# Optimization experiments

Hardware: AMD Instinct MI355X
Metric: run time of the kernel (lower is better)

The kernel has to match this reference:

```python
import jax, jax.numpy as jnp
import numpy as np

D = 1280          # hidden_size
NH = 16           # num_heads
HD = 80           # head_dim
DEPTH = 4         # number of vision blocks
INTER = 3420      # mlp intermediate size
MERGE = 2         # spatial_merge_size
OUT = 3584        # merger out_hidden_size
GRID = (1, 40, 40)  # (t, h, w) patch grid -> 1600 tokens
N = GRID[0] * GRID[1] * GRID[2]
PATCH_IN = 3 * 2 * 14 * 14  # in_channels * temporal_patch * patch^2 = 1176


def _pos_emb():
    """Deterministic vision RoPE cos/sin per Qwen2_5_VLVisionModel.rot_pos_emb."""
    t, h, w = GRID
    mh, mw = h // MERGE, w // MERGE
    intra = np.arange(MERGE)
    row = np.arange(mh)[:, None, None, None] * MERGE + intra[None, None, :, None]
    col = np.arange(mw)[None, :, None, None] * MERGE + intra[None, None, None, :]
    row = np.broadcast_to(row, (mh, mw, MERGE, MERGE)).reshape(-1)
    col = np.broadcast_to(col, (mh, mw, MERGE, MERGE)).reshape(-1)
    pos = np.stack([row, col], axis=-1)        # (h*w, 2)
    if t > 1:
        pos = np.tile(pos, (t, 1))
    rot_dim = HD // 2                          # 40
    inv = 1.0 / (10000.0 ** (np.arange(0, rot_dim, 2, dtype=np.float64) / rot_dim))
    table = np.outer(np.arange(max(h, w)), inv)        # (max_hw, rot_dim//2)
    rpe = table[pos].reshape(pos.shape[0], -1)         # (N, rot_dim)
    emb = np.concatenate([rpe, rpe], axis=-1)          # (N, HD)
    return np.cos(emb).astype(np.float32), np.sin(emb).astype(np.float32)


def setup_inputs() -> dict:
    key = jax.random.key(0)
    ks = iter(jax.random.split(key, 40))
    def w(shape, s=0.02):
        return jax.random.normal(next(ks), shape, jnp.float32) * s
    cos, sin = _pos_emb()
    return dict(
        pixel_values=w((N, PATCH_IN), 1.0),
        cos=jnp.asarray(cos), sin=jnp.asarray(sin),
        patch_w=w((D, PATCH_IN)),                       # Conv3d stride==kernel -> linear
        norm1_w=jnp.ones((DEPTH, D), jnp.float32),
        qkv_w=w((DEPTH, 3 * D, D)), qkv_b=jnp.zeros((DEPTH, 3 * D), jnp.float32),
        proj_w=w((DEPTH, D, D)), proj_b=jnp.zeros((DEPTH, D), jnp.float32),
        norm2_w=jnp.ones((DEPTH, D), jnp.float32),
        gate_w=w((DEPTH, INTER, D)), gate_b=jnp.zeros((DEPTH, INTER), jnp.float32),
        up_w=w((DEPTH, INTER, D)), up_b=jnp.zeros((DEPTH, INTER), jnp.float32),
        down_w=w((DEPTH, D, INTER)), down_b=jnp.zeros((DEPTH, D), jnp.float32),
        lnq_w=jnp.ones((D,), jnp.float32),
        m1_w=w((D * MERGE ** 2, D * MERGE ** 2)), m1_b=jnp.zeros((D * MERGE ** 2,), jnp.float32),
        m2_w=w((OUT, D * MERGE ** 2)), m2_b=jnp.zeros((OUT,), jnp.float32),
    )


def _rms(x, w, eps=1e-6):
    return x * jax.lax.rsqrt(jnp.mean(x * x, axis=-1, keepdims=True) + eps) * w


def _rotate_half(x):
    x1, x2 = jnp.split(x, 2, axis=-1)
    return jnp.concatenate([-x2, x1], axis=-1)


def _forward(pixel_values, cos, sin, patch_w, norm1_w, qkv_w, qkv_b, proj_w, proj_b,
             norm2_w, gate_w, gate_b, up_w, up_b, down_w, down_b,
             lnq_w, m1_w, m1_b, m2_w, m2_b):
    # patch embed: Conv3d with kernel==stride collapses to a linear projection
    x = pixel_values @ patch_w.T                       # (N, D)
    c = cos[:, None, :]                                # (N, 1, HD)
    s = sin[:, None, :]
    scale = HD ** -0.5
    for i in range(DEPTH):
        # --- attention ---
        h = _rms(x, norm1_w[i])
        qkv = (h @ qkv_w[i].T + qkv_b[i]).reshape(N, 3, NH, HD)
        q, k, v = qkv[:, 0], qkv[:, 1], qkv[:, 2]      # (N, NH, HD)
        q = q * c + _rotate_half(q) * s
        k = k * c + _rotate_half(k) * s
        # NOTE: this impl applies NO cu_seqlens window mask -> full dense attention
        aw = jnp.einsum('nhd,mhd->hnm', q, k) * scale  # (NH, N, N)
        aw = jax.nn.softmax(aw.astype(jnp.float32), axis=-1).astype(x.dtype)
        o = jnp.einsum('hnm,mhd->nhd', aw, v).reshape(N, D)
        x = x + o @ proj_w[i].T + proj_b[i]
        # --- mlp (SwiGLU) ---
        h = _rms(x, norm2_w[i])
        g = h @ gate_w[i].T + gate_b[i]
        u = h @ up_w[i].T + up_b[i]
        x = x + (jax.nn.silu(g) * u) @ down_w[i].T + down_b[i]
    # --- patch merger ---
    h = _rms(x, lnq_w).reshape(-1, D * MERGE ** 2)      # (N/4, 5120)
    h = jax.nn.gelu(h @ m1_w.T + m1_b, approximate=False)
    return h @ m2_w.T + m2_b                            # (N/4, OUT)


def reference(pixel_values, cos, sin, patch_w, norm1_w, qkv_w, qkv_b, proj_w, proj_b,
              norm2_w, gate_w, gate_b, up_w, up_b, down_w, down_b,
              lnq_w, m1_w, m1_b, m2_w, m2_b):
    return _forward(pixel_values, cos, sin, patch_w, norm1_w, qkv_w, qkv_b, proj_w,
                    proj_b, norm2_w, gate_w, gate_b, up_w, up_b, down_w, down_b,
                    lnq_w, m1_w, m1_b, m2_w, m2_b)
```

## Files before the change

### kernel.cpp

```cpp
#include <hip/hip_runtime.h>


typedef __bf16 bf16x8 __attribute__((ext_vector_type(8)));
typedef float  f32x4  __attribute__((ext_vector_type(4)));
typedef unsigned short u16;

#define DEV __device__ __forceinline__

DEV u16 f2bf(float f) {
    union { float f; unsigned u; } v; v.f = f;
    unsigned r = v.u + 0x7FFFu + ((v.u >> 16) & 1u);
    return (u16)(r >> 16);
}
DEV float bf2f(u16 b) {
    union { float f; unsigned u; } v; v.u = ((unsigned)b) << 16; return v.f;
}

DEV void gload16(const u16* g, u16* l) {
    __builtin_amdgcn_global_load_lds(
        (const __attribute__((address_space(1))) unsigned int*)g,
        (__attribute__((address_space(3))) unsigned int*)l, 16, 0, 0);
}

enum { EPI_NONE = 0, EPI_BIAS = 1, EPI_BIAS_RESID = 2, EPI_BIAS_GELU = 3, EPI_PART = 4 };

DEV unsigned xcd_map(unsigned lin, unsigned nwg) {
    unsigned q = nwg >> 3, r = nwg & 7, xc = lin & 7, off = lin >> 3;
    return (xc < r ? xc * (q + 1) : r * (q + 1) + (xc - r) * q) + off;
}

__global__ void cvt_kernel(const float* __restrict__ src, u16* __restrict__ dst,
                           int Rs, int Cs, int Rp, int Cp,
                           long long sls, long long dls)
{
    const float* s = src + (size_t)blockIdx.y * sls;
    u16* d = dst + (size_t)blockIdx.y * dls;
    int idx = blockIdx.x * 256 + threadIdx.x;
    int cpc = Cp >> 3;
    if (idx >= Rp * cpc) return;
    int row = idx / cpc;
    int c0  = (idx - row * cpc) * 8;
    u16 v[8];
    if (row < Rs && c0 + 8 <= Cs) {
        float4 a = *reinterpret_cast<const float4*>(&s[(size_t)row * Cs + c0]);
        float4 b = *reinterpret_cast<const float4*>(&s[(size_t)row * Cs + c0 + 4]);
        v[0] = f2bf(a.x); v[1] = f2bf(a.y); v[2] = f2bf(a.z); v[3] = f2bf(a.w);
        v[4] = f2bf(b.x); v[5] = f2bf(b.y); v[6] = f2bf(b.z); v[7] = f2bf(b.w);
    } else {
#pragma unroll
        for (int j = 0; j < 8; ++j) {
            int c = c0 + j;
            v[j] = (row < Rs && c < Cs) ? f2bf(s[(size_t)row * Cs + c]) : (u16)0;
        }
    }
    *reinterpret_cast<uint4*>(&d[(size_t)row * Cp + c0]) =
        *reinterpret_cast<const uint4*>(v);
}

__global__ void gub_kernel(const float* __restrict__ gb, const float* __restrict__ ub,
                           float* __restrict__ dst)
{
    int i = blockIdx.x * 256 + threadIdx.x;
    if (i >= 4 * 6912) return;
    int l = i / 6912, c = i - l * 6912;
    float v = 0.f;
    if (c < 3456) { if (c < 3420) v = gb[l * 3420 + c]; }
    else { int c2 = c - 3456; if (c2 < 3420) v = ub[l * 3420 + c2]; }
    dst[i] = v;
}

template <int EPI, bool OF32>
__global__ __launch_bounds__(256, 3)
void gemm16_kernel(const u16* __restrict__ A, const u16* __restrict__ B,
                   const float* __restrict__ bias, const float* __restrict__ resid,
                   void* __restrict__ outp, int Kp, int ldc, int Rlim,
                   int ktn, size_t zstride)
{
    __shared__ u16 sA[3][4096];
    __shared__ u16 sB[3][4096];
    const int tid  = threadIdx.x;
    const int lane = tid & 63;
    const int w    = tid >> 6;

    const unsigned gy  = gridDim.y;
    const unsigned nwg = gridDim.x * gy;
    const unsigned lin = blockIdx.x + blockIdx.y * gridDim.x;
    const unsigned id2 = xcd_map(lin, nwg);
    const int c0 = (int)(id2 / gy) * 128;
    const int r0 = (int)(id2 - (id2 / gy) * gy) * 128;

    const int wr  = (w >> 1) * 64;
    const int wc  = (w & 1) * 64;
    const int l15 = lane & 15;
    const int kk  = (lane >> 4) * 8;
    const int pco = (((lane >> 4) ^ ((l15 >> 1) & 3)) * 8) - kk;

    const int ca  = w * 128 + lane;
    const int cb  = ca + 64;
    const int sza = ((ca & 3) ^ ((ca >> 3) & 3)) * 8;
    const int szb = ((cb & 3) ^ ((cb >> 3) & 3)) * 8;
    const size_t arow0 = (size_t)(r0 + (ca >> 2)) * Kp + sza;
    const size_t brow0 = (size_t)(c0 + (ca >> 2)) * Kp + sza;
    const size_t arow1 = (size_t)(r0 + (cb >> 2)) * Kp + szb;
    const size_t brow1 = (size_t)(c0 + (cb >> 2)) * Kp + szb;

    f32x4 acc[4][4];
#pragma unroll
    for (int i = 0; i < 4; ++i)
#pragma unroll
        for (int j = 0; j < 4; ++j) acc[i][j] = (f32x4){0.f, 0.f, 0.f, 0.f};

    const int kt0 = blockIdx.z * ktn;
    auto stage = [&](int kt, int buf) {
        int k0 = kt * 32;
        gload16(A + arow0 + k0, &sA[buf][ca * 8]);
        gload16(B + brow0 + k0, &sB[buf][ca * 8]);
        gload16(A + arow1 + k0, &sA[buf][cb * 8]);
        gload16(B + brow1 + k0, &sB[buf][cb * 8]);
    };
    auto compute = [&](int buf) {
        bf16x8 af[4], bfr[4];
#pragma unroll
        for (int f = 0; f < 4; ++f) {
            af[f]  = *reinterpret_cast<const bf16x8*>(&sA[buf][(wr + f * 16 + l15) * 32 + kk + pco]);
            bfr[f] = *reinterpret_cast<const bf16x8*>(&sB[buf][(wc + f * 16 + l15) * 32 + kk + pco]);
        }
#pragma unroll
        for (int fr = 0; fr < 4; ++fr)
#pragma unroll
            for (int fc = 0; fc < 4; ++fc)
                acc[fr][fc] = __builtin_amdgcn_mfma_f32_16x16x32_bf16(af[fr], bfr[fc], acc[fr][fc], 0, 0, 0);
    };

    const int NT = ktn;
    stage(kt0, 0);
    if (NT > 1) stage(kt0 + 1, 1);
    int bcur = 0;
    for (int t = 0; t < NT - 1; ++t) {
        asm volatile("s_waitcnt vmcnt(4)" ::: "memory");
        __builtin_amdgcn_s_barrier();
        __builtin_amdgcn_sched_barrier(0);
        if (t + 2 < NT) {
            int bn = bcur + 2; if (bn >= 3) bn -= 3;
            stage(kt0 + t + 2, bn);
        }
        __builtin_amdgcn_sched_barrier(0);
        compute(bcur);
        bcur = (bcur == 2) ? 0 : bcur + 1;
    }
    asm volatile("s_waitcnt vmcnt(0)" ::: "memory");
    __builtin_amdgcn_s_barrier();
    __builtin_amdgcn_sched_barrier(0);
    compute(bcur);

    const int rowb = r0 + wr + (lane >> 4) * 4;
    const int colb = c0 + wc + l15;
    if (EPI == EPI_PART) {
        float* pp = (float*)outp + (size_t)blockIdx.z * zstride;
#pragma unroll
        for (int fc = 0; fc < 4; ++fc) {
            int col = colb + fc * 16;
#pragma unroll
            for (int fr = 0; fr < 4; ++fr)
#pragma unroll
                for (int r2 = 0; r2 < 4; ++r2)
                    pp[(size_t)(rowb + fr * 16 + r2) * ldc + col] = acc[fr][fc][r2];
        }
        return;
    }
#pragma unroll
    for (int fc = 0; fc < 4; ++fc) {
        int col = colb + fc * 16;
        float bv = (EPI != EPI_NONE) ? bias[col] : 0.f;
#pragma unroll
        for (int fr = 0; fr < 4; ++fr) {
#pragma unroll
            for (int r2 = 0; r2 < 4; ++r2) {
                int row = rowb + fr * 16 + r2;
                if (row >= Rlim) continue;
                float v = acc[fr][fc][r2] + bv;
                if (EPI == EPI_BIAS_RESID) v += resid[(size_t)row * ldc + col];
                if (EPI == EPI_BIAS_GELU)  v = 0.5f * v * (1.f + erff(v * 0.70710678118f));
                if (OF32) ((float*)outp)[(size_t)row * ldc + col] = v;
                else      ((u16*)outp)[(size_t)row * ldc + col] = f2bf(v);
            }
        }
    }
}

template <int EPI, bool OF32>
__global__ __launch_bounds__(256, 4)
void gemm32_kernel(const u16* __restrict__ A, const u16* __restrict__ B,
                   const float* __restrict__ bias, const float* __restrict__ resid,
                   void* __restrict__ outp, int Kp, int ldc, int Rlim)
{
    __shared__ u16 sA[3][1024];
    __shared__ u16 sB[3][4096];
    const int tid  = threadIdx.x;
    const int lane = tid & 63;
    const int w    = tid >> 6;

    const unsigned gy  = gridDim.y;
    const unsigned nwg = gridDim.x * gy;
    const unsigned lin = blockIdx.x + blockIdx.y * gridDim.x;
    const unsigned id2 = xcd_map(lin, nwg);
    const int c0 = (int)(id2 / gy) * 128;
    const int r0 = (int)(id2 - (id2 / gy) * gy) * 32;

    const int wc  = w * 32;
    const int l15 = lane & 15;
    const int kk  = (lane >> 4) * 8;
    const int pco = (((lane >> 4) ^ ((l15 >> 1) & 3)) * 8) - kk;

    const int cB0 = tid, cB1 = tid + 256, cA = tid & 127;
    const size_t bsrc0 = (size_t)(c0 + (cB0 >> 2)) * Kp + ((cB0 & 3) ^ ((cB0 >> 3) & 3)) * 8;
    const size_t bsrc1 = (size_t)(c0 + (cB1 >> 2)) * Kp + ((cB1 & 3) ^ ((cB1 >> 3) & 3)) * 8;
    const size_t asrc  = (size_t)(r0 + (cA  >> 2)) * Kp + ((cA  & 3) ^ ((cA  >> 3) & 3)) * 8;

    f32x4 acc[2][2];
#pragma unroll
    for (int i = 0; i < 2; ++i)
#pragma unroll
        for (int j = 0; j < 2; ++j) acc[i][j] = (f32x4){0.f, 0.f, 0.f, 0.f};

    auto stage = [&](int kt, int buf) {
        int k0 = kt * 32;
        gload16(B + bsrc0 + k0, &sB[buf][cB0 * 8]);
        gload16(B + bsrc1 + k0, &sB[buf][cB1 * 8]);
        gload16(A + asrc  + k0, &sA[buf][cA * 8]);
    };
    auto compute = [&](int buf) {
        bf16x8 af[2], bfr[2];
#pragma unroll
        for (int f = 0; f < 2; ++f) {
            af[f]  = *reinterpret_cast<const bf16x8*>(&sA[buf][(f * 16 + l15) * 32 + kk + pco]);
            bfr[f] = *reinterpret_cast<const bf16x8*>(&sB[buf][(wc + f * 16 + l15) * 32 + kk + pco]);
        }
#pragma unroll
        for (int fr = 0; fr < 2; ++fr)
#pragma unroll
            for (int fc = 0; fc < 2; ++fc)
                acc[fr][fc] = __builtin_amdgcn_mfma_f32_16x16x32_bf16(af[fr], bfr[fc], acc[fr][fc], 0, 0, 0);
    };

    const int NT = Kp >> 5;
    stage(0, 0);
    stage(1, 1);
    int bcur = 0;
    for (int t = 0; t < NT - 1; ++t) {
        asm volatile("s_waitcnt vmcnt(3)" ::: "memory");
        __builtin_amdgcn_s_barrier();
        __builtin_amdgcn_sched_barrier(0);
        if (t + 2 < NT) {
            int bn = bcur + 2; if (bn >= 3) bn -= 3;
            stage(t + 2, bn);
        }
        __builtin_amdgcn_sched_barrier(0);
        compute(bcur);
        bcur = (bcur == 2) ? 0 : bcur + 1;
    }
    asm volatile("s_waitcnt vmcnt(0)" ::: "memory");
    __builtin_amdgcn_s_barrier();
    __builtin_amdgcn_sched_barrier(0);
    compute(bcur);

    const int rowb = r0 + (lane >> 4) * 4;
    const int colb = c0 + wc + l15;
#pragma unroll
    for (int fc = 0; fc < 2; ++fc) {
        int col = colb + fc * 16;
        float bv = (EPI != EPI_NONE) ? bias[col] : 0.f;
#pragma unroll
        for (int fr = 0; fr < 2; ++fr) {
#pragma unroll
            for (int r2 = 0; r2 < 4; ++r2) {
                int row = rowb + fr * 16 + r2;
                if (row >= Rlim) continue;
                float v = acc[fr][fc][r2] + bv;
                if (EPI == EPI_BIAS_RESID) v += resid[(size_t)row * ldc + col];
                if (EPI == EPI_BIAS_GELU)  v = 0.5f * v * (1.f + erff(v * 0.70710678118f));
                if (OF32) ((float*)outp)[(size_t)row * ldc + col] = v;
                else      ((u16*)outp)[(size_t)row * ldc + col] = f2bf(v);
            }
        }
    }
}

template <int GELU, bool OF32>
__global__ void reduce_kernel(const float* __restrict__ part, const float* __restrict__ bias,
                              void* __restrict__ outp, int C, int S, size_t zstride, int total4)
{
    int i = blockIdx.x * 256 + threadIdx.x;
    if (i >= total4) return;
    int cq = C >> 2;
    int rr = i / cq;
    int cc = (i - rr * cq) * 4;
    size_t bidx = (size_t)rr * C + cc;
    float4 s = *reinterpret_cast<const float4*>(&part[bidx]);
    for (int z = 1; z < S; ++z) {
        float4 p = *reinterpret_cast<const float4*>(&part[z * zstride + bidx]);
        s.x += p.x; s.y += p.y; s.z += p.z; s.w += p.w;
    }
    float4 b = *reinterpret_cast<const float4*>(&bias[cc]);
    s.x += b.x; s.y += b.y; s.z += b.z; s.w += b.w;
    if (GELU) {
        s.x = 0.5f * s.x * (1.f + erff(s.x * 0.70710678118f));
        s.y = 0.5f * s.y * (1.f + erff(s.y * 0.70710678118f));
        s.z = 0.5f * s.z * (1.f + erff(s.z * 0.70710678118f));
        s.w = 0.5f * s.w * (1.f + erff(s.w * 0.70710678118f));
    }
    if (OF32) {
        *reinterpret_cast<float4*>(&((float*)outp)[bidx]) = s;
    } else {
        u16 v[4] = { f2bf(s.x), f2bf(s.y), f2bf(s.z), f2bf(s.w) };
        *reinterpret_cast<uint2*>(&((u16*)outp)[bidx]) = *reinterpret_cast<const uint2*>(v);
    }
}

__global__ void rms_kernel(const float* __restrict__ x, const float* __restrict__ w,
                           u16* __restrict__ out, int cols)
{
    const int row = blockIdx.x;
    const int tid = threadIdx.x;
    const float* xr = x + (size_t)row * cols;
    float ss = 0.f;
    for (int c = tid; c < cols; c += 256) { float v = xr[c]; ss += v * v; }
#pragma unroll
    for (int m = 1; m < 64; m <<= 1) ss += __shfl_xor(ss, m);
    __shared__ float wsum[4];
    if ((tid & 63) == 0) wsum[tid >> 6] = ss;
    __syncthreads();
    float tot = wsum[0] + wsum[1] + wsum[2] + wsum[3];
    float rs = rsqrtf(tot / (float)cols + 1e-6f);
    u16* orow = out + (size_t)row * cols;
    for (int c = tid; c < cols; c += 256) orow[c] = f2bf(xr[c] * rs * w[c]);
}

__global__ void rope_kernel(u16* __restrict__ qkv, const float* __restrict__ cosb,
                            const float* __restrict__ sinb)
{
    int idx = blockIdx.x * 256 + threadIdx.x;
    int n   = idx / 640;
    int rem = idx - n * 640;
    int hh  = rem / 40;
    int d   = rem - hh * 40;
    float c0 = cosb[n * 80 + d];
    float s0 = sinb[n * 80 + d];
    float c1 = cosb[n * 80 + d + 40];
    float s1 = sinb[n * 80 + d + 40];
    size_t base = (size_t)n * 3840 + hh * 80;
    float a = bf2f(qkv[base + d]), b = bf2f(qkv[base + d + 40]);
    qkv[base + d]      = f2bf(a * c0 - b * s0);
    qkv[base + d + 40] = f2bf(b * c1 + a * s1);
    base += 1280;
    a = bf2f(qkv[base + d]); b = bf2f(qkv[base + d + 40]);
    qkv[base + d]      = f2bf(a * c0 - b * s0);
    qkv[base + d + 40] = f2bf(b * c1 + a * s1);
}

__global__ void silu_mul_kernel(const u16* __restrict__ gu, u16* __restrict__ outb)
{
    int idx = blockIdx.x * 256 + threadIdx.x;
    if (idx >= 1664 * 432) return;
    int row = idx / 432, c8 = (idx - row * 432) * 8;
    u16 gv[8], uv[8];
    *reinterpret_cast<uint4*>(gv) = *reinterpret_cast<const uint4*>(&gu[(size_t)row * 6912 + c8]);
    *reinterpret_cast<uint4*>(uv) = *reinterpret_cast<const uint4*>(&gu[(size_t)row * 6912 + 3456 + c8]);
#pragma unroll
    for (int j = 0; j < 8; ++j) {
        float x = bf2f(gv[j]);
        gv[j] = f2bf(x / (1.f + expf(-x)) * bf2f(uv[j]));
    }
    *reinterpret_cast<uint4*>(&outb[(size_t)row * 3456 + c8]) = *reinterpret_cast<const uint4*>(gv);
}

__global__ __launch_bounds__(256, 2)
void attn_kernel(const u16* __restrict__ qkv, u16* __restrict__ o)
{
    __shared__ __align__(16) u16 Klds[64][104];
    __shared__ __align__(16) u16 Vt[80][72];
    __shared__ __align__(16) u16 Plds[4][16][72];
    const int tid  = threadIdx.x;
    const int lane = tid & 63;
    const int w    = tid >> 6;
    const int l15  = lane & 15;
    const int kk   = (lane >> 4) * 8;
    unsigned lin = blockIdx.y * 25 + blockIdx.x;
    unsigned id2 = (lin & 7) * 50 + (lin >> 3);
    const int hh = (int)(id2 / 25);
    const int qt = (int)(id2 - hh * 25);
    const float scale = 0.11180339887498949f;

    const int qrow = qt * 64 + w * 16 + l15;
    bf16x8 aq[3];
#pragma unroll
    for (int s = 0; s < 3; ++s) {
        int d = 32 * s + kk;
        union { bf16x8 v; uint4 q; } uu;
        if (d < 80) uu.q = *reinterpret_cast<const uint4*>(&qkv[(size_t)qrow * 3840 + hh * 80 + d]);
        else        uu.q = (uint4){0u, 0u, 0u, 0u};
        aq[s] = uu.v;
    }

    f32x4 acc_o[5];
#pragma unroll
    for (int fd = 0; fd < 5; ++fd) acc_o[fd] = (f32x4){0.f, 0.f, 0.f, 0.f};
    float m[4], lsum[4];
#pragma unroll
    for (int r2 = 0; r2 < 4; ++r2) { m[r2] = -__builtin_inff(); lsum[r2] = 0.f; }

    const int koff = 1280 + hh * 80;
    const int voff = 2560 + hh * 80;

    for (int kb = 0; kb < 25; ++kb) {
#pragma unroll
        for (int i = 0; i < 3; ++i) {
            int c = tid + 256 * i;
            int r = c / 12, c8 = (c - r * 12) * 8;
            uint4 pk = (uint4){0u, 0u, 0u, 0u};
            if (c8 < 80)
                pk = *reinterpret_cast<const uint4*>(&qkv[(size_t)(kb * 64 + r) * 3840 + koff + c8]);
            *reinterpret_cast<uint4*>(&Klds[r][c8]) = pk;
        }
#pragma unroll
        for (int i = 0; i < 3; ++i) {
            int c = tid + 256 * i;
            if (c < 640) {
                int r = c / 10, c8 = (c - r * 10) * 8;
                u16 v[8];
                *reinterpret_cast<uint4*>(v) =
                    *reinterpret_cast<const uint4*>(&qkv[(size_t)(kb * 64 + r) * 3840 + voff + c8]);
#pragma unroll
                for (int j = 0; j < 8; ++j) Vt[c8 + j][r] = v[j];
            }
        }
        __syncthreads();

        f32x4 sf[4];
#pragma unroll
        for (int fc = 0; fc < 4; ++fc) {
            f32x4 c = (f32x4){0.f, 0.f, 0.f, 0.f};
#pragma unroll
            for (int s = 0; s < 3; ++s)
                c = __builtin_amdgcn_mfma_f32_16x16x32_bf16(
                        aq[s],
                        *reinterpret_cast<const bf16x8*>(&Klds[fc * 16 + l15][32 * s + kk]),
                        c, 0, 0, 0);
            sf[fc] = c * scale;
        }

        float mx[4];
#pragma unroll
        for (int r2 = 0; r2 < 4; ++r2)
            mx[r2] = fmaxf(fmaxf(sf[0][r2], sf[1][r2]), fmaxf(sf[2][r2], sf[3][r2]));
#pragma unroll
        for (int msk = 1; msk <= 8; msk <<= 1)
#pragma unroll
            for (int r2 = 0; r2 < 4; ++r2)
                mx[r2] = fmaxf(mx[r2], __shfl_xor(mx[r2], msk));
        float alpha[4];
#pragma unroll
        for (int r2 = 0; r2 < 4; ++r2) {
            float mn = fmaxf(m[r2], mx[r2]);
            alpha[r2] = expf(m[r2] - mn);
            m[r2] = mn;
        }
        float psum[4] = {0.f, 0.f, 0.f, 0.f};
#pragma unroll
        for (int fc = 0; fc < 4; ++fc)
#pragma unroll
            for (int r2 = 0; r2 < 4; ++r2) {
                float p = expf(sf[fc][r2] - m[r2]);
                sf[fc][r2] = p;
                psum[r2] += p;
            }
#pragma unroll
        for (int msk = 1; msk <= 8; msk <<= 1)
#pragma unroll
            for (int r2 = 0; r2 < 4; ++r2) psum[r2] += __shfl_xor(psum[r2], msk);
#pragma unroll
        for (int r2 = 0; r2 < 4; ++r2) lsum[r2] = lsum[r2] * alpha[r2] + psum[r2];
#pragma unroll
        for (int fd = 0; fd < 5; ++fd)
#pragma unroll
            for (int r2 = 0; r2 < 4; ++r2) acc_o[fd][r2] *= alpha[r2];

        const int prow = (lane >> 4) * 4;
#pragma unroll
        for (int fc = 0; fc < 4; ++fc)
#pragma unroll
            for (int r2 = 0; r2 < 4; ++r2)
                Plds[w][prow + r2][fc * 16 + l15] = f2bf(sf[fc][r2]);

        bf16x8 ap[2];
#pragma unroll
        for (int ks = 0; ks < 2; ++ks)
            ap[ks] = *reinterpret_cast<const bf16x8*>(&Plds[w][l15][32 * ks + kk]);
#pragma unroll
        for (int fd = 0; fd < 5; ++fd)
#pragma unroll
            for (int ks = 0; ks < 2; ++ks)
                acc_o[fd] = __builtin_amdgcn_mfma_f32_16x16x32_bf16(
                        ap[ks],
                        *reinterpret_cast<const bf16x8*>(&Vt[fd * 16 + l15][32 * ks + kk]),
                        acc_o[fd], 0, 0, 0);
        __syncthreads();
    }

    float inv[4];
#pragma unroll
    for (int r2 = 0; r2 < 4; ++r2) inv[r2] = 1.f / lsum[r2];
    const int orow = qt * 64 + w * 16 + (lane >> 4) * 4;
    const int ocol = hh * 80 + l15;
#pragma unroll
    for (int fd = 0; fd < 5; ++fd)
#pragma unroll
        for (int r2 = 0; r2 < 4; ++r2)
            o[(size_t)(orow + r2) * 1280 + ocol + fd * 16] = f2bf(acc_o[fd][r2] * inv[r2]);
}

extern "C" void kernel_launch(void* const* d_in, const int* in_sizes, int n_in,
                              void* d_out, int out_size, void* d_ws, size_t ws_size,
                              hipStream_t stream)
{
    const float* pixel  = (const float*)d_in[0];
    const float* cosb   = (const float*)d_in[1];
    const float* sinb   = (const float*)d_in[2];
    const float* patchw = (const float*)d_in[3];
    const float* n1w    = (const float*)d_in[4];
    const float* qkvw   = (const float*)d_in[5];
    const float* qkvb   = (const float*)d_in[6];
    const float* projw  = (const float*)d_in[7];
    const float* projb  = (const float*)d_in[8];
    const float* n2w    = (const float*)d_in[9];
    const float* gatew  = (const float*)d_in[10];
    const float* gateb  = (const float*)d_in[11];
    const float* upw    = (const float*)d_in[12];
    const float* upb    = (const float*)d_in[13];
    const float* downw  = (const float*)d_in[14];
    const float* downb  = (const float*)d_in[15];
    const float* lnqw   = (const float*)d_in[16];
    const float* m1w    = (const float*)d_in[17];
    const float* m1b    = (const float*)d_in[18];
    const float* m2w    = (const float*)d_in[19];
    const float* m2b    = (const float*)d_in[20];
    float* out = (float*)d_out;

    char* base = (char*)d_ws;
    float* x      = (float*)(base);
    u16*   h      = (u16*)(base + 8519680);
    u16*   qbuf   = (u16*)(base + 12779520);
    u16*   pix16  = qbuf;
    u16*   gsep   = (u16*)(base + 25559040);
    u16*   o      = gsep;
    u16*   pw16   = gsep;
    u16*   gu     = (u16*)(base + 37060608);
    u16*   t1     = gu;
    float* guB    = (float*)(base + 60063744);
    u16*   qkvw16 = (u16*)(base + 60174336);
    u16*   projw16= (u16*)(base + 99495936);
    u16*   guw16  = (u16*)(base + 112603136);
    u16*   downw16= (u16*)(base + 183382016);
    u16*   m1w16  = guw16;
    u16*   m2w16  = (u16*)(base + 112603136 + 52428800);
    float* part   = (float*)qkvw16;

    dim3 blk(256);
    auto cvb = [](int Rp, int Cp) { return (Rp * (Cp >> 3) + 255) / 256; };

    cvt_kernel<<<dim3(cvb(1664,1216),1), blk, 0, stream>>>(pixel, pix16, 1600, 1176, 1664, 1216, 0, 0);
    cvt_kernel<<<dim3(cvb(1280,1216),1), blk, 0, stream>>>(patchw, pw16, 1280, 1176, 1280, 1216, 0, 0);
    cvt_kernel<<<dim3(cvb(15360,1280),1), blk, 0, stream>>>(qkvw, qkvw16, 15360, 1280, 15360, 1280, 0, 0);
    cvt_kernel<<<dim3(cvb(5120,1280),1), blk, 0, stream>>>(projw, projw16, 5120, 1280, 5120, 1280, 0, 0);
    cvt_kernel<<<dim3(cvb(3456,1280),4), blk, 0, stream>>>(gatew, guw16, 3420, 1280, 3456, 1280, 4377600LL, 8847360LL);
    cvt_kernel<<<dim3(cvb(3456,1280),4), blk, 0, stream>>>(upw, guw16 + 4423680, 3420, 1280, 3456, 1280, 4377600LL, 8847360LL);
    cvt_kernel<<<dim3(cvb(1280,3456),4), blk, 0, stream>>>(downw, downw16, 1280, 3420, 1280, 3456, 4377600LL, 4423680LL);
    gub_kernel<<<108, blk, 0, stream>>>(gateb, upb, guB);

    gemm32_kernel<EPI_NONE, true><<<dim3(10,52), blk, 0, stream>>>(pix16, pw16, nullptr, nullptr, x, 1216, 1280, 1664);
    for (int i = 0; i < 4; ++i) {
        rms_kernel<<<1600, blk, 0, stream>>>(x, n1w + i*1280, h, 1280);
        gemm16_kernel<EPI_BIAS, false><<<dim3(30,13), blk, 0, stream>>>(h, qkvw16 + (size_t)i*4915200, qkvb + i*3840, nullptr, qbuf, 1280, 3840, 1664, 40, 0);
        rope_kernel<<<4000, blk, 0, stream>>>(qbuf, cosb, sinb);
        attn_kernel<<<dim3(25,16), blk, 0, stream>>>(qbuf, o);
        gemm32_kernel<EPI_BIAS_RESID, true><<<dim3(10,52), blk, 0, stream>>>(o, projw16 + (size_t)i*1638400, projb + i*1280, x, x, 1280, 1280, 1664);
        rms_kernel<<<1600, blk, 0, stream>>>(x, n2w + i*1280, h, 1280);
        gemm16_kernel<EPI_BIAS, false><<<dim3(54,13), blk, 0, stream>>>(h, guw16 + (size_t)i*8847360, guB + i*6912, nullptr, gu, 1280, 6912, 1664, 40, 0);
        silu_mul_kernel<<<2808, blk, 0, stream>>>(gu, gsep);
        gemm16_kernel<EPI_BIAS_RESID, true><<<dim3(10,13), blk, 0, stream>>>(gsep, downw16 + (size_t)i*4423680, downb + i*1280, x, x, 3456, 1280, 1664, 108, 0);
    }
    cvt_kernel<<<dim3(cvb(5120,5120),1), blk, 0, stream>>>(m1w, m1w16, 5120, 5120, 5120, 5120, 0, 0);
    cvt_kernel<<<dim3(cvb(3584,5120),1), blk, 0, stream>>>(m2w, m2w16, 3584, 5120, 3584, 5120, 0, 0);
    rms_kernel<<<1600, blk, 0, stream>>>(x, lnqw, h, 1280);
    gemm16_kernel<EPI_PART, false><<<dim3(40,4,5), blk, 0, stream>>>(h, m1w16, nullptr, nullptr, part, 5120, 5120, 512, 32, 2621440);
    reduce_kernel<1, false><<<2560, blk, 0, stream>>>(part, m1b, t1, 5120, 5, 2621440, 655360);
    gemm16_kernel<EPI_PART, false><<<dim3(28,4,5), blk, 0, stream>>>(t1, m2w16, nullptr, nullptr, part, 5120, 3584, 512, 32, 1835008);
    reduce_kernel<0, true><<<1400, blk, 0, stream>>>(part, m2b, out, 3584, 5, 1835008, 358400);
}
```

Measured before the change: 1.564 ms.

## Double-buffer K/V tiles in attention with register prefetch and packed V transpose

Attention now keeps two LDS buffers for K and V. The next tile's global loads go into registers before the current tile's compute and are written to the other buffer afterwards, leaving one barrier per iteration instead of two. This hides global load latency behind the MFMA work. The V transpose now packs pairs of rows into 32-bit LDS writes to cut the number of scalar 16-bit stores. expf is swapped for __expf in the softmax and SiLU. In exchange, LDS use and register pressure go up, which may lower occupancy.

```diff
diff --git a/kernel.cpp b/kernel.cpp
--- a/kernel.cpp
+++ b/kernel.cpp
@@ -369,7 +369,7 @@
 #pragma unroll
     for (int j = 0; j < 8; ++j) {
         float x = bf2f(gv[j]);
-        gv[j] = f2bf(x / (1.f + expf(-x)) * bf2f(uv[j]));
+        gv[j] = f2bf(x / (1.f + __expf(-x)) * bf2f(uv[j]));
     }
     *reinterpret_cast<uint4*>(&outb[(size_t)row * 3456 + c8]) = *reinterpret_cast<const uint4*>(gv);
 }
@@ -377,9 +377,9 @@
 __global__ __launch_bounds__(256, 2)
 void attn_kernel(const u16* __restrict__ qkv, u16* __restrict__ o)
 {
-    __shared__ __align__(16) u16 Klds[64][104];
-    __shared__ __align__(16) u16 Vt[80][72];
-    __shared__ __align__(16) u16 Plds[4][16][72];
+    __shared__ __align__(16) u16      Klds[2][64][104];
+    __shared__ __align__(16) unsigned Vt32[2][80][36];
+    __shared__ __align__(16) u16      Plds[4][16][72];
     const int tid  = threadIdx.x;
     const int lane = tid & 63;
     const int w    = tid >> 6;
@@ -391,6 +391,16 @@
     const int qt = (int)(id2 - hh * 25);
     const float scale = 0.11180339887498949f;
 
+    const int koff = 1280 + hh * 80;
+    const int voff = 2560 + hh * 80;
+
+    {
+        int r  = tid >> 2;
+        int cq = 80 + (tid & 3) * 4;
+        *reinterpret_cast<uint2*>(&Klds[0][r][cq]) = make_uint2(0u, 0u);
+        *reinterpret_cast<uint2*>(&Klds[1][r][cq]) = make_uint2(0u, 0u);
+    }
+
     const int qrow = qt * 64 + w * 16 + l15;
     bf16x8 aq[3];
 #pragma unroll
@@ -398,9 +408,52 @@
         int d = 32 * s + kk;
         union { bf16x8 v; uint4 q; } uu;
         if (d < 80) uu.q = *reinterpret_cast<const uint4*>(&qkv[(size_t)qrow * 3840 + hh * 80 + d]);
-        else        uu.q = (uint4){0u, 0u, 0u, 0u};
+        else        uu.q = make_uint4(0u, 0u, 0u, 0u);
         aq[s] = uu.v;
     }
+
+    const int kc0 = tid, kc1 = tid + 256, kc2 = tid + 512;
+    const int kr0 = kc0 / 10, k80 = (kc0 - kr0 * 10) * 8;
+    const int kr1 = kc1 / 10, k81 = (kc1 - kr1 * 10) * 8;
+    const int kr2 = kc2 / 10, k82 = (kc2 - kr2 * 10) * 8;
+    const size_t ksrc0 = (size_t)kr0 * 3840 + koff + k80;
+    const size_t ksrc1 = (size_t)kr1 * 3840 + koff + k81;
+    const size_t ksrc2 = (size_t)kr2 * 3840 + koff + k82;
+    const int rpA = tid & 31, gA = tid >> 5;
+    const int gB = 8 + (tid >> 5);
+    const size_t vsrcA = (size_t)(2 * rpA) * 3840 + voff + gA * 8;
+    const size_t vsrcB = (size_t)(2 * rpA) * 3840 + voff + gB * 8;
+
+    uint4 kg0, kg1, kg2, va0, va1, vb0, vb1;
+    auto LOADR = [&](int kb) {
+        size_t tb = (size_t)kb * 245760;
+        kg0 = *reinterpret_cast<const uint4*>(&qkv[tb + ksrc0]);
+        kg1 = *reinterpret_cast<const uint4*>(&qkv[tb + ksrc1]);
+        if (tid < 128) kg2 = *reinterpret_cast<const uint4*>(&qkv[tb + ksrc2]);
+        va0 = *reinterpret_cast<const uint4*>(&qkv[tb + vsrcA]);
+        va1 = *reinterpret_cast<const uint4*>(&qkv[tb + vsrcA + 3840]);
+        if (tid < 64) {
+            vb0 = *reinterpret_cast<const uint4*>(&qkv[tb + vsrcB]);
+            vb1 = *reinterpret_cast<const uint4*>(&qkv[tb + vsrcB + 3840]);
+        }
+    };
+    auto STORE = [&](int b) {
+        *reinterpret_cast<uint4*>(&Klds[b][kr0][k80]) = kg0;
+        *reinterpret_cast<uint4*>(&Klds[b][kr1][k81]) = kg1;
+        if (tid < 128) *reinterpret_cast<uint4*>(&Klds[b][kr2][k82]) = kg2;
+        union { uint4 q; u16 h[8]; } xa0, xa1;
+        xa0.q = va0; xa1.q = va1;
+#pragma unroll
+        for (int j = 0; j < 8; ++j)
+            Vt32[b][gA * 8 + j][rpA] = (unsigned)xa0.h[j] | ((unsigned)xa1.h[j] << 16);
+        if (tid < 64) {
+            union { uint4 q; u16 h[8]; } xb0, xb1;
+            xb0.q = vb0; xb1.q = vb1;
+#pragma unroll
+            for (int j = 0; j < 8; ++j)
+                Vt32[b][gB * 8 + j][rpA] = (unsigned)xb0.h[j] | ((unsigned)xb1.h[j] << 16);
+        }
+    };
 
     f32x4 acc_o[5];
 #pragma unroll
@@ -409,32 +462,13 @@
 #pragma unroll
     for (int r2 = 0; r2 < 4; ++r2) { m[r2] = -__builtin_inff(); lsum[r2] = 0.f; }
 
-    const int koff = 1280 + hh * 80;
-    const int voff = 2560 + hh * 80;
+    LOADR(0);
+    STORE(0);
+    __syncthreads();
+    int cur = 0;
 
     for (int kb = 0; kb < 25; ++kb) {
-#pragma unroll
-        for (int i = 0; i < 3; ++i) {
-            int c = tid + 256 * i;
-            int r = c / 12, c8 = (c - r * 12) * 8;
-            uint4 pk = (uint4){0u, 0u, 0u, 0u};
-            if (c8 < 80)
-                pk = *reinterpret_cast<const uint4*>(&qkv[(size_t)(kb * 64 + r) * 3840 + koff + c8]);
-            *reinterpret_cast<uint4*>(&Klds[r][c8]) = pk;
-        }
-#pragma unroll
-        for (int i = 0; i < 3; ++i) {
-            int c = tid + 256 * i;
-            if (c < 640) {
-                int r = c / 10, c8 = (c - r * 10) * 8;
-                u16 v[8];
-                *reinterpret_cast<uint4*>(v) =
-                    *reinterpret_cast<const uint4*>(&qkv[(size_t)(kb * 64 + r) * 3840 + voff + c8]);
-#pragma unroll
-                for (int j = 0; j < 8; ++j) Vt[c8 + j][r] = v[j];
-            }
-        }
-        __syncthreads();
+        if (kb < 24) LOADR(kb + 1);
 
         f32x4 sf[4];
 #pragma unroll
@@ -444,7 +478,7 @@
             for (int s = 0; s < 3; ++s)
                 c = __builtin_amdgcn_mfma_f32_16x16x32_bf16(
                         aq[s],
-                        *reinterpret_cast<const bf16x8*>(&Klds[fc * 16 + l15][32 * s + kk]),
+                        *reinterpret_cast<const bf16x8*>(&Klds[cur][fc * 16 + l15][32 * s + kk]),
                         c, 0, 0, 0);
             sf[fc] = c * scale;
         }
@@ -462,7 +496,7 @@
 #pragma unroll
         for (int r2 = 0; r2 < 4; ++r2) {
             float mn = fmaxf(m[r2], mx[r2]);
-            alpha[r2] = expf(m[r2] - mn);
+            alpha[r2] = __expf(m[r2] - mn);
             m[r2] = mn;
         }
         float psum[4] = {0.f, 0.f, 0.f, 0.f};
@@ -470,7 +504,7 @@
         for (int fc = 0; fc < 4; ++fc)
 #pragma unroll
             for (int r2 = 0; r2 < 4; ++r2) {
-                float p = expf(sf[fc][r2] - m[r2]);
+                float p = __expf(sf[fc][r2] - m[r2]);
                 sf[fc][r2] = p;
                 psum[r2] += p;
             }
@@ -497,14 +531,19 @@
         for (int ks = 0; ks < 2; ++ks)
             ap[ks] = *reinterpret_cast<const bf16x8*>(&Plds[w][l15][32 * ks + kk]);
 #pragma unroll
-        for (int fd = 0; fd < 5; ++fd)
+        for (int fd = 0; fd < 5; ++fd) {
+            const u16* vrow = reinterpret_cast<const u16*>(&Vt32[cur][fd * 16 + l15][0]);
 #pragma unroll
             for (int ks = 0; ks < 2; ++ks)
                 acc_o[fd] = __builtin_amdgcn_mfma_f32_16x16x32_bf16(
                         ap[ks],
-                        *reinterpret_cast<const bf16x8*>(&Vt[fd * 16 + l15][32 * ks + kk]),
+                        *reinterpret_cast<const bf16x8*>(&vrow[32 * ks + kk]),
                         acc_o[fd], 0, 0, 0);
+        }
+
+        if (kb < 24) STORE(cur ^ 1);
         __syncthreads();
+        cur ^= 1;
     }
 
     float inv[4];
```

Result: faster. 1.399 ms (-10.5%).
